# Optimization experiments

Measured on AMD Instinct MI355X. Metric: run time of the kernel, lower is better.

The kernel has to match this reference:

```python
import jax, jax.numpy as jnp
import numpy as np

N, E, B = 131072, 262144, 4096
NODE_DIM, EDGE_DIM, HIDDEN = 16, 4, 64
MLP_HID = 128


def setup_inputs() -> dict:
    key = jax.random.key(0)
    ks = jax.random.split(key, 16)
    def nrm(k, shape, s=0.05):
        return jax.random.normal(k, shape, jnp.float32) * s
    return {
        "x": jax.random.normal(ks[0], (N, NODE_DIM), jnp.float32),
        "edge_attr": jax.random.normal(ks[1], (E, EDGE_DIM), jnp.float32),
        "edge_index": jax.random.randint(ks[2], (2, E), 0, N),
        "batch": jnp.sort(jax.random.randint(ks[3], (N,), 0, B)),
        "w_e1": nrm(ks[4], (EDGE_DIM, MLP_HID)),
        "b_e1": jnp.zeros((MLP_HID,), jnp.float32),
        "w_e2": nrm(ks[5], (MLP_HID, NODE_DIM * HIDDEN)),
        "b_e2": jnp.zeros((NODE_DIM * HIDDEN,), jnp.float32),
        "root": nrm(ks[6], (NODE_DIM, HIDDEN)),
        "conv_bias": jnp.zeros((HIDDEN,), jnp.float32),
        "gru_wih": nrm(ks[7], (3 * HIDDEN, HIDDEN)),
        "gru_whh": nrm(ks[8], (3 * HIDDEN, HIDDEN)),
        "gru_bih": jnp.zeros((3 * HIDDEN,), jnp.float32),
        "gru_bhh": jnp.zeros((3 * HIDDEN,), jnp.float32),
        "lstm_wih": nrm(ks[9], (4 * HIDDEN, 2 * HIDDEN)),
        "lstm_whh": nrm(ks[10], (4 * HIDDEN, HIDDEN)),
        "lstm_bih": jnp.zeros((4 * HIDDEN,), jnp.float32),
        "lstm_bhh": jnp.zeros((4 * HIDDEN,), jnp.float32),
        "fc1_w": nrm(ks[11], (2 * HIDDEN, HIDDEN)),
        "fc1_b": jnp.zeros((HIDDEN,), jnp.float32),
        "fc2_w": nrm(ks[12], (HIDDEN, 1)),
        "fc2_b": jnp.zeros((1,), jnp.float32),
    }


def reference(x, edge_attr, edge_index, batch,
              w_e1, b_e1, w_e2, b_e2, root, conv_bias,
              gru_wih, gru_whh, gru_bih, gru_bhh,
              lstm_wih, lstm_whh, lstm_bih, lstm_bhh,
              fc1_w, fc1_b, fc2_w, fc2_b):
    src, dst = edge_index[0], edge_index[1]
    # NNConv: edge-MLP -> per-edge weight [E, node_dim, hidden]
    Wdyn = (jax.nn.relu(edge_attr @ w_e1 + b_e1) @ w_e2 + b_e2).reshape(E, NODE_DIM, HIDDEN)
    msg = jnp.einsum('ed,edh->eh', x[src], Wdyn)  # gather + per-edge matmul
    msum = jax.ops.segment_sum(msg, dst, num_segments=N)
    cnt = jax.ops.segment_sum(jnp.ones((E,), msg.dtype), dst, num_segments=N)
    agg = msum / jnp.maximum(cnt, 1.0)[:, None]  # scatter-mean
    out = jax.nn.relu(agg + x @ root + conv_bias)
    h = out
    for _ in range(3):
        gi = out @ gru_wih.T + gru_bih
        gh = h @ gru_whh.T + gru_bhh
        ir, iz, inn = jnp.split(gi, 3, axis=-1)
        hr, hz, hn = jnp.split(gh, 3, axis=-1)
        r = jax.nn.sigmoid(ir + hr)
        z = jax.nn.sigmoid(iz + hz)
        n = jnp.tanh(inn + r * hn)
        h = (1.0 - z) * n + z * h
        out = h
    # Set2Set, 3 processing steps
    hl = jnp.zeros((B, HIDDEN), out.dtype)
    cl = jnp.zeros((B, HIDDEN), out.dtype)
    q_star = jnp.zeros((B, 2 * HIDDEN), out.dtype)
    for _ in range(3):
        gates = q_star @ lstm_wih.T + lstm_bih + hl @ lstm_whh.T + lstm_bhh
        ig, fg, gg, og = jnp.split(gates, 4, axis=-1)
        ig = jax.nn.sigmoid(ig); fg = jax.nn.sigmoid(fg)
        gg = jnp.tanh(gg); og = jax.nn.sigmoid(og)
        cl = fg * cl + ig * gg
        hl = og * jnp.tanh(cl)
        q = hl  # [B, H]
        e = jnp.sum(out * q[batch], axis=-1)  # [N]
        m = jax.lax.stop_gradient(jax.ops.segment_max(e, batch, num_segments=B))
        ex = jnp.exp(e - m[batch])
        denom = jax.ops.segment_sum(ex, batch, num_segments=B)
        a = ex / denom[batch]  # segment softmax
        r_g = jax.ops.segment_sum(a[:, None] * out, batch, num_segments=B)
        q_star = jnp.concatenate([q, r_g], axis=-1)
    y = jax.nn.relu(q_star @ fc1_w + fc1_b)
    return (y @ fc2_w + fc2_b).squeeze(-1)
```

## Files before the change

### kernel.cpp

```cpp
#include <hip/hip_runtime.h>
#include <math.h>

#define N_NODES 131072
#define N_EDGES 262144
#define N_B     4096

typedef __attribute__((ext_vector_type(8))) short short8;
typedef __attribute__((ext_vector_type(8))) _Float16 half8;
typedef __attribute__((ext_vector_type(4))) float f32x4;
typedef __attribute__((ext_vector_type(16))) float f32x16;

__device__ __forceinline__ float fast_sig(float x) {
    return 1.0f / (1.0f + __expf(-x));
}
__device__ __forceinline__ float fast_tanh(float x) {
    float t = __expf(-2.0f * fabsf(x));
    float r = (1.0f - t) / (1.0f + t);
    return copysignf(r, x);
}

__device__ __forceinline__ void split_fp16(float v, _Float16& hi, _Float16& lo) {
    _Float16 h = (_Float16)v;
    hi = h;
    lo = (_Float16)(v - (float)h);
}

__global__ __launch_bounds__(256) void k_misc(
    const float* __restrict__ we2, unsigned short* __restrict__ wt,
    const float* __restrict__ gwih, const float* __restrict__ gwhh,
    const float* __restrict__ gbih, const float* __restrict__ gbhh,
    unsigned short* __restrict__ wtg, float* __restrict__ gbias,
    const float* __restrict__ lwih, const float* __restrict__ lwhh,
    float4* __restrict__ wA, float4* __restrict__ wB,
    const int* __restrict__ batch, int* __restrict__ starts,
    const int* __restrict__ eidx, int* __restrict__ deg)
{
    const int bid = blockIdx.x;
    const int tid = threadIdx.x;
    if (bid >= 105) {
        int p = (bid - 105) * 256 + tid;
        atomicAdd(&deg[eidx[N_EDGES + p]], 1);
        return;
    }
    if (bid < 64) {
        int p = bid * 256 + tid;
        int d = p >> 10;
        int u = (p >> 9) & 1;
        int s = (p >> 6) & 7;
        int l = p & 63;
        int k0 = s * 16 + ((l >> 5) << 3);
        int h = u * 32 + (l & 31);
        half8 hv;
        #pragma unroll
        for (int j = 0; j < 8; ++j) {
            float v = we2[(size_t)(k0 + j) * 1024 + d * 64 + h];
            hv[j] = (_Float16)v;
        }
        size_t base = (size_t)d * 8192 + (size_t)u * 4096 + s * 512 + l * 8;
        *(half8*)&wt[base] = hv;
    } else if (bid < 72) {
        int p = (bid - 64) * 256 + tid;
        if (p < 256) {
            int g = p >> 6, j = p & 63;
            float b;
            if (g == 0)      b = gbih[j] + gbhh[j];
            else if (g == 1) b = gbih[64 + j] + gbhh[64 + j];
            else if (g == 2) b = gbih[128 + j];
            else             b = gbhh[128 + j];
            gbias[p] = b;
        }
        int u = p >> 7, ks = (p >> 6) & 1, ln = p & 63;
        int n = u * 16 + (ln & 15);
        int g = n >> 6, jn = n & 63;
        int k0 = ks * 32 + (ln >> 4) * 8;
        half8 hv;
        #pragma unroll
        for (int jj = 0; jj < 8; ++jj) {
            int k = k0 + jj;
            float v;
            if (g == 0)      v = gwih[jn * 64 + k] + gwhh[jn * 64 + k];
            else if (g == 1) v = gwih[(64 + jn) * 64 + k] + gwhh[(64 + jn) * 64 + k];
            else if (g == 2) v = gwih[(128 + jn) * 64 + k];
            else             v = gwhh[(128 + jn) * 64 + k];
            hv[jj] = (_Float16)v;
        }
        size_t base = (size_t)(u * 2 + ks) * 512 + ln * 8;
        *(half8*)&wtg[base] = hv;
    } else if (bid < 88) {
        int p = (bid - 72) * 256 + tid;
        int k = p >> 6, ln = p & 63;
        float4 a, b;
        a.x = lwih[(0 * 64 + ln) * 128 + k] + lwhh[(0 * 64 + ln) * 64 + k];
        a.y = lwih[(1 * 64 + ln) * 128 + k] + lwhh[(1 * 64 + ln) * 64 + k];
        a.z = lwih[(2 * 64 + ln) * 128 + k] + lwhh[(2 * 64 + ln) * 64 + k];
        a.w = lwih[(3 * 64 + ln) * 128 + k] + lwhh[(3 * 64 + ln) * 64 + k];
        b.x = lwih[(0 * 64 + ln) * 128 + 64 + k];
        b.y = lwih[(1 * 64 + ln) * 128 + 64 + k];
        b.z = lwih[(2 * 64 + ln) * 128 + 64 + k];
        b.w = lwih[(3 * 64 + ln) * 128 + 64 + k];
        wA[p] = a; wB[p] = b;
    } else {
        int g = (bid - 88) * 256 + tid;
        if (g > N_B) return;
        if (g == N_B) { starts[N_B] = N_NODES; return; }
        int lo = 0, hi = N_NODES;
        while (lo < hi) {
            int mid = (lo + hi) >> 1;
            if (batch[mid] < g) lo = mid + 1; else hi = mid;
        }
        starts[g] = lo;
    }
}

__global__ __launch_bounds__(256) void k_scan1(
    const int* __restrict__ deg, int* __restrict__ psum)
{
    __shared__ int sm[256];
    const int t = threadIdx.x;
    sm[t] = deg[blockIdx.x * 256 + t];
    __syncthreads();
    #pragma unroll
    for (int off = 128; off; off >>= 1) {
        if (t < off) sm[t] += sm[t + off];
        __syncthreads();
    }
    if (t == 0) psum[blockIdx.x] = sm[0];
}

__global__ __launch_bounds__(512) void k_scan2(
    const int* __restrict__ psum, int* __restrict__ psumx)
{
    __shared__ int sm[512];
    const int t = threadIdx.x;
    sm[t] = psum[t];
    __syncthreads();
    #pragma unroll
    for (int off = 1; off < 512; off <<= 1) {
        int add = (t >= off) ? sm[t - off] : 0;
        __syncthreads();
        sm[t] += add;
        __syncthreads();
    }
    psumx[t] = (t > 0) ? sm[t - 1] : 0;
}

__global__ __launch_bounds__(256) void k_scan3(
    const int* __restrict__ deg, const int* __restrict__ psumx,
    int* __restrict__ row_ptr, int* __restrict__ cursor)
{
    __shared__ int sm[256];
    const int t = threadIdx.x;
    const int i = blockIdx.x * 256 + t;
    int d = deg[i];
    sm[t] = d;
    __syncthreads();
    #pragma unroll
    for (int off = 1; off < 256; off <<= 1) {
        int add = (t >= off) ? sm[t - off] : 0;
        __syncthreads();
        sm[t] += add;
        __syncthreads();
    }
    int excl = sm[t] - d + psumx[blockIdx.x];
    row_ptr[i] = excl;
    cursor[i] = excl;
    if (i == 0) row_ptr[N_NODES] = N_EDGES;
}

__global__ __launch_bounds__(256) void k_scat(
    const int* __restrict__ eidx, int* __restrict__ cursor,
    int* __restrict__ epos)
{
    int e = blockIdx.x * 256 + threadIdx.x;
    int dst = eidx[N_EDGES + e];
    epos[e] = atomicAdd(&cursor[dst], 1);
}

__global__ __launch_bounds__(512)
__attribute__((amdgpu_waves_per_eu(4, 8)))
void k_edge(
    const float* __restrict__ x,
    const float* __restrict__ ea,
    const int*   __restrict__ eidx,
    const int*   __restrict__ epos,
    const float* __restrict__ we1,
    const float* __restrict__ be1,
    const unsigned short* __restrict__ wt,
    const float* __restrict__ be2,
    float* __restrict__ emsg)
{
    __shared__ unsigned short sAh[16384];
    __shared__ float sxT[16 * 136];
    __shared__ float sbe2[1024];
    __shared__ int   spos[128];

    const int tid = threadIdx.x;
    const int w   = tid >> 6;
    const int ln  = tid & 63;
    const int u   = w >> 2;
    const int mt  = w & 3;
    const int eb  = blockIdx.x * 128;

    if (tid < 128) spos[tid] = epos[eb + tid];
    #pragma unroll
    for (int v = tid; v < 1024; v += 512) sbe2[v] = be2[v];

    {
        int e = tid >> 2, q = tid & 3;
        int src = eidx[eb + e];
        float4 t4 = ((const float4*)(x + (size_t)src * 16))[q];
        sxT[(q * 4 + 0) * 136 + e] = t4.x;
        sxT[(q * 4 + 1) * 136 + e] = t4.y;
        sxT[(q * 4 + 2) * 136 + e] = t4.z;
        sxT[(q * 4 + 3) * 136 + e] = t4.w;
    }

    #pragma unroll 1
    for (int i = 0; i < 4; ++i) {
        int cc = tid + i * 512;
        int mtc = cc >> 9;
        int s  = (cc >> 6) & 7;
        int l  = cc & 63;
        int e   = mtc * 32 + (l & 31);
        int kk0 = s * 16 + ((l >> 5) << 3);
        float4 eav = *(const float4*)(ea + (size_t)(eb + e) * 4);
        float4 b0 = *(const float4*)(be1 + kk0);
        float4 b1 = *(const float4*)(be1 + kk0 + 4);
        float acc[8] = {b0.x, b0.y, b0.z, b0.w, b1.x, b1.y, b1.z, b1.w};
        #pragma unroll
        for (int a = 0; a < 4; ++a) {
            float4 wa0 = *(const float4*)(we1 + a * 128 + kk0);
            float4 wa1 = *(const float4*)(we1 + a * 128 + kk0 + 4);
            float ev = (a == 0) ? eav.x : (a == 1) ? eav.y : (a == 2) ? eav.z : eav.w;
            acc[0] += ev * wa0.x; acc[1] += ev * wa0.y;
            acc[2] += ev * wa0.z; acc[3] += ev * wa0.w;
            acc[4] += ev * wa1.x; acc[5] += ev * wa1.y;
            acc[6] += ev * wa1.z; acc[7] += ev * wa1.w;
        }
        half8 hv;
        #pragma unroll
        for (int j = 0; j < 8; ++j) {
            hv[j] = (_Float16)fmaxf(acc[j], 0.0f);
        }
        *(half8*)&sAh[cc * 8] = hv;
    }
    __syncthreads();

    half8 ah[8];
    #pragma unroll
    for (int s = 0; s < 8; ++s) {
        ah[s] = *(half8*)&sAh[((mt * 8 + s) * 64 + ln) * 8];
    }
    #pragma unroll
    for (int s = 0; s < 8; ++s) {
        asm volatile("" : "+v"(ah[s]));
    }

    const unsigned short* wdu = wt + (size_t)u * 4096;
    const int d0 = blockIdx.x & 15;
    const int rbase = (ln >> 5) * 4;

    f32x16 msg;
    #pragma unroll
    for (int r = 0; r < 16; ++r) msg[r] = 0.0f;

    half8 bq[8];
    {
        const unsigned short* p0 = wdu + (size_t)d0 * 8192 + ln * 8;
        #pragma unroll
        for (int f = 0; f < 7; ++f) bq[f] = *(const half8*)(p0 + f * 512);
    }

    #pragma unroll 1
    for (int dd = 0; dd < 16; ++dd) {
        const int d = (d0 + dd) & 15;
        const unsigned short* wd  = wdu + (size_t)d * 8192;
        const unsigned short* wnx = wdu + (size_t)((d + 1) & 15) * 8192;

        float bv = sbe2[d * 64 + u * 32 + (ln & 31)];
        f32x16 c2;
        #pragma unroll
        for (int r = 0; r < 16; ++r) c2[r] = bv;

        #pragma unroll
        for (int s = 0; s < 8; ++s) {
            if (s == 0) {
                bq[7] = *(const half8*)(wd + 7 * 512 + ln * 8);
            } else if (dd < 15) {
                bq[s - 1] = *(const half8*)(wnx + (s - 1) * 512 + ln * 8);
            }
            c2 = __builtin_amdgcn_mfma_f32_32x32x16_f16(ah[s], bq[s], c2, 0, 0, 0);
        }
        #pragma unroll
        for (int q = 0; q < 4; ++q) {
            f32x4 xv = *(const f32x4*)&sxT[d * 136 + mt * 32 + rbase + 8 * q];
            #pragma unroll
            for (int j = 0; j < 4; ++j) {
                msg[q * 4 + j] = fmaf(xv[j], c2[q * 4 + j], msg[q * 4 + j]);
            }
        }
    }

    const int col = u * 32 + (ln & 31);
    #pragma unroll
    for (int r = 0; r < 16; ++r) {
        int row = (r & 3) + ((r >> 2) * 8) + rbase;
        int pos = spos[mt * 32 + row];
        emsg[(size_t)pos * 64 + col] = msg[r];
    }
}

__global__ __launch_bounds__(256, 2) void k_gru2(
    float* __restrict__ buf,
    const float* __restrict__ emsg,
    const int* __restrict__ rowp,
    const float* __restrict__ x,
    const float* __restrict__ root,
    const float* __restrict__ cb,
    const unsigned short* __restrict__ wtg,
    const float* __restrict__ gbias)
{
    __shared__ unsigned short sAh[16384];
    __shared__ unsigned short sAl[16384];
    __shared__ float sroot[1024];
    __shared__ float sbias[256];
    __shared__ float scb[64];
    const int tid = threadIdx.x;
    const int w = tid >> 6, ln = tid & 63, lq = ln >> 4, lm = ln & 15;
    const size_t nbase = (size_t)blockIdx.x * 256;

    #pragma unroll
    for (int v = tid; v < 1024; v += 256) sroot[v] = root[v];
    sbias[tid] = gbias[tid];
    if (tid < 64) scb[tid] = cb[tid];
    __syncthreads();

    #pragma unroll 2
    for (int i = 0; i < 8; ++i) {
        int cc = tid + i * 256;
        int mt = cc >> 7, ks = (cc >> 6) & 1, l = cc & 63;
        size_t gn = nbase + mt * 16 + (l & 15);
        int c0 = ks * 32 + (l >> 4) * 8;
        int rp0 = rowp[gn], rp1 = rowp[gn + 1];
        float ms[8] = {0.f, 0.f, 0.f, 0.f, 0.f, 0.f, 0.f, 0.f};
        for (int k = rp0; k < rp1; ++k) {
            float4 m0 = *(const float4*)(emsg + (size_t)k * 64 + c0);
            float4 m1 = *(const float4*)(emsg + (size_t)k * 64 + c0 + 4);
            ms[0] += m0.x; ms[1] += m0.y; ms[2] += m0.z; ms[3] += m0.w;
            ms[4] += m1.x; ms[5] += m1.y; ms[6] += m1.z; ms[7] += m1.w;
        }
        float cinv = 1.0f / fmaxf((float)(rp1 - rp0), 1.0f);
        float xv[16];
        *(float4*)&xv[0]  = *(const float4*)(x + gn * 16);
        *(float4*)&xv[4]  = *(const float4*)(x + gn * 16 + 4);
        *(float4*)&xv[8]  = *(const float4*)(x + gn * 16 + 8);
        *(float4*)&xv[12] = *(const float4*)(x + gn * 16 + 12);
        float acc[8];
        #pragma unroll
        for (int j = 0; j < 8; ++j) acc[j] = scb[c0 + j];
        #pragma unroll
        for (int d = 0; d < 16; ++d) {
            float xd = xv[d];
            #pragma unroll
            for (int j = 0; j < 8; ++j) acc[j] += xd * sroot[d * 64 + c0 + j];
        }
        half8 hv, lv;
        #pragma unroll
        for (int j = 0; j < 8; ++j) {
            float hval = fmaxf(ms[j] * cinv + acc[j], 0.0f);
            _Float16 hi, lo; split_fp16(hval, hi, lo);
            hv[j] = hi; lv[j] = lo;
        }
        *(half8*)&sAh[cc * 8] = hv;
        *(half8*)&sAl[cc * 8] = lv;
    }
    __syncthreads();

    #pragma unroll 1
    for (int step = 0; step < 3; ++step) {
        half8 ah[4][2], al[4][2];
        #pragma unroll
        for (int i = 0; i < 4; ++i)
            #pragma unroll
            for (int ks = 0; ks < 2; ++ks) {
                int mt = w * 4 + i;
                ah[i][ks] = *(half8*)&sAh[((mt * 2 + ks) * 64 + ln) * 8];
                al[i][ks] = *(half8*)&sAl[((mt * 2 + ks) * 64 + ln) * 8];
            }
        __syncthreads();

        #pragma unroll 1
        for (int v = 0; v < 4; ++v) {
            f32x4 C[4][4];
            #pragma unroll
            for (int g = 0; g < 4; ++g) {
                float bv = sbias[g * 64 + v * 16 + lm];
                #pragma unroll
                for (int i = 0; i < 4; ++i) C[g][i] = (f32x4){bv, bv, bv, bv};
            }
            #pragma unroll
            for (int g = 0; g < 4; ++g) {
                int u = g * 4 + v;
                #pragma unroll
                for (int ks = 0; ks < 2; ++ks) {
                    size_t wb = (size_t)(u * 2 + ks) * 512 + ln * 8;
                    half8 bb = *(const half8*)&wtg[wb];
                    #pragma unroll
                    for (int i = 0; i < 4; ++i) {
                        C[g][i] = __builtin_amdgcn_mfma_f32_16x16x32_f16(ah[i][ks], bb, C[g][i], 0, 0, 0);
                        C[g][i] = __builtin_amdgcn_mfma_f32_16x16x32_f16(al[i][ks], bb, C[g][i], 0, 0, 0);
                    }
                }
            }
            int ksp = v >> 1;
            int lq2 = (v & 1) * 2 + (lm >> 3);
            int jp = lm & 7;
            #pragma unroll
            for (int i = 0; i < 4; ++i) {
                int mt = w * 4 + i;
                #pragma unroll
                for (int r = 0; r < 4; ++r) {
                    int idx = ((mt * 2 + ksp) * 64 + lq2 * 16 + lq * 4 + r) * 8 + jp;
                    float hold = (float)*(const _Float16*)&sAh[idx]
                               + (float)*(const _Float16*)&sAl[idx];
                    float rr = fast_sig(C[0][i][r]);
                    float zz = fast_sig(C[1][i][r]);
                    float nn = fast_tanh(C[2][i][r] + rr * C[3][i][r]);
                    float hnew = (1.0f - zz) * nn + zz * hold;
                    if (step < 2) {
                        _Float16 hi, lo; split_fp16(hnew, hi, lo);
                        sAh[idx] = *(unsigned short*)&hi;
                        sAl[idx] = *(unsigned short*)&lo;
                    } else {
                        buf[(nbase + mt * 16 + lq * 4 + r) * 64 + v * 16 + lm] = hnew;
                    }
                }
            }
        }
        if (step < 2) __syncthreads();
    }
}

__global__ __launch_bounds__(256) void k_s2s(
    const float* __restrict__ out,
    const int*   __restrict__ starts,
    const float4* __restrict__ wA,
    const float4* __restrict__ wB,
    const float* __restrict__ bih,
    const float* __restrict__ bhh,
    const float* __restrict__ fc1w,
    const float* __restrict__ fc1b,
    const float* __restrict__ fc2w,
    const float* __restrict__ fc2b,
    float* __restrict__ y)
{
    __shared__ float osh[4][32][66];
    __shared__ float qsL[4][128];
    __shared__ float ebuf[4][256];
    const int tid = threadIdx.x;
    const int wv = tid >> 6, ln = tid & 63;
    const int gid = blockIdx.x * 4 + wv;

    const int s0 = starts[gid];
    int L = starts[gid + 1] - s0; if (L > 256) L = 256;
    const int SL = (L < 32) ? L : 32;

    #pragma unroll
    for (int base = 0; base < 32; base += 4) {
        int row = base + (ln >> 4);
        int c4 = (ln & 15) * 4;
        if (row < SL)
            *(float4*)&osh[wv][row][c4] =
                *(const float4*)(out + (size_t)(s0 + row) * 64 + c4);
    }

    qsL[wv][ln] = 0.0f; qsL[wv][64 + ln] = 0.0f;
    __builtin_amdgcn_wave_barrier();

    const float b0 = bih[ln] + bhh[ln];
    const float b1 = bih[64 + ln] + bhh[64 + ln];
    const float b2 = bih[128 + ln] + bhh[128 + ln];
    const float b3 = bih[192 + ln] + bhh[192 + ln];

    float c = 0.0f;

    #pragma unroll 1
    for (int step = 0; step < 3; ++step) {
        float a0 = b0, a1 = b1, a2 = b2, a3 = b3;
        #pragma unroll 4
        for (int k = 0; k < 64; ++k) {
            float qk = qsL[wv][k];
            float rk = qsL[wv][64 + k];
            float4 wa = wA[k * 64 + ln];
            float4 wb = wB[k * 64 + ln];
            a0 += wa.x * qk + wb.x * rk;
            a1 += wa.y * qk + wb.y * rk;
            a2 += wa.z * qk + wb.z * rk;
            a3 += wa.w * qk + wb.w * rk;
        }
        float ig = fast_sig(a0), fg = fast_sig(a1);
        float gg = fast_tanh(a2), og = fast_sig(a3);
        c = fg * c + ig * gg;
        float h = og * fast_tanh(c);
        __builtin_amdgcn_wave_barrier();
        qsL[wv][ln] = h;
        __builtin_amdgcn_wave_barrier();

        float m = -1e30f;
        for (int c0 = 0; c0 * 64 < L; ++c0) {
            int j = c0 * 64 + ln;
            if (j < L) {
                float a = 0.0f;
                if (j < SL) {
                    #pragma unroll
                    for (int l4 = 0; l4 < 16; ++l4) {
                        float4 ov = *(const float4*)&osh[wv][j][l4 * 4];
                        float4 hv = *(const float4*)&qsL[wv][l4 * 4];
                        a += ov.x * hv.x + ov.y * hv.y + ov.z * hv.z + ov.w * hv.w;
                    }
                } else {
                    const float4* orow = (const float4*)(out + (size_t)(s0 + j) * 64);
                    #pragma unroll
                    for (int l4 = 0; l4 < 16; ++l4) {
                        float4 ov = orow[l4];
                        float4 hv = *(const float4*)&qsL[wv][l4 * 4];
                        a += ov.x * hv.x + ov.y * hv.y + ov.z * hv.z + ov.w * hv.w;
                    }
                }
                ebuf[wv][j] = a;
                m = fmaxf(m, a);
            }
        }
        #pragma unroll
        for (int off = 32; off; off >>= 1) m = fmaxf(m, __shfl_xor(m, off));
        float ds = 0.0f;
        for (int c0 = 0; c0 * 64 < L; ++c0) {
            int j = c0 * 64 + ln;
            if (j < L) {
                float ex = __expf(ebuf[wv][j] - m);
                ebuf[wv][j] = ex;
                ds += ex;
            }
        }
        #pragma unroll
        for (int off = 32; off; off >>= 1) ds += __shfl_xor(ds, off);
        __builtin_amdgcn_wave_barrier();
        float rg = 0.0f;
        for (int j = 0; j < SL; ++j)
            rg = fmaf(ebuf[wv][j], osh[wv][j][ln], rg);
        for (int j = SL; j < L; ++j)
            rg = fmaf(ebuf[wv][j], out[(size_t)(s0 + j) * 64 + ln], rg);
        rg = (L > 0) ? (rg / ds) : 0.0f;
        qsL[wv][64 + ln] = rg;
        __builtin_amdgcn_wave_barrier();
    }

    float a = fc1b[ln];
    #pragma unroll 4
    for (int k = 0; k < 128; ++k)
        a = fmaf(qsL[wv][k], fc1w[k * 64 + ln], a);
    float uu = fmaxf(a, 0.0f) * fc2w[ln];
    #pragma unroll
    for (int off = 32; off; off >>= 1) uu += __shfl_xor(uu, off);
    if (ln == 0) y[gid] = uu + fc2b[0];
}

extern "C" void kernel_launch(void* const* d_in, const int* in_sizes, int n_in,
                              void* d_out, int out_size, void* d_ws, size_t ws_size,
                              hipStream_t stream) {
    const float* x     = (const float*)d_in[0];
    const float* ea    = (const float*)d_in[1];
    const int*   eidx  = (const int*)d_in[2];
    const int*   batch = (const int*)d_in[3];
    const float* we1   = (const float*)d_in[4];
    const float* be1   = (const float*)d_in[5];
    const float* we2   = (const float*)d_in[6];
    const float* be2   = (const float*)d_in[7];
    const float* root  = (const float*)d_in[8];
    const float* cb    = (const float*)d_in[9];
    const float* gwih  = (const float*)d_in[10];
    const float* gwhh  = (const float*)d_in[11];
    const float* gbih  = (const float*)d_in[12];
    const float* gbhh  = (const float*)d_in[13];
    const float* lwih  = (const float*)d_in[14];
    const float* lwhh  = (const float*)d_in[15];
    const float* lbih  = (const float*)d_in[16];
    const float* lbhh  = (const float*)d_in[17];
    const float* fc1w  = (const float*)d_in[18];
    const float* fc1b  = (const float*)d_in[19];
    const float* fc2w  = (const float*)d_in[20];
    const float* fc2b  = (const float*)d_in[21];

    float* emsg = (float*)d_ws;
    float* buf  = emsg + (size_t)N_EDGES * 64;
    int* deg    = (int*)(buf + (size_t)N_NODES * 64);
    int* cursor = deg + N_NODES;
    int* rowp   = cursor + N_NODES;
    int* epos   = rowp + N_NODES + 1;
    int* psum   = epos + N_EDGES;
    int* psumx  = psum + 512;
    int* starts = psumx + 512;
    size_t off = (size_t)((char*)(starts + N_B + 1) - (char*)d_ws);
    off = (off + 15) & ~(size_t)15;
    unsigned short* wt  = (unsigned short*)((char*)d_ws + off);
    unsigned short* wtg = wt + 262144;
    float* gbias = (float*)(wtg + 32768);
    float4* wA = (float4*)(gbias + 256);
    float4* wB = wA + 4096;
    float* y = (float*)d_out;

    hipMemsetAsync(deg, 0, (size_t)N_NODES * sizeof(int), stream);
    k_misc<<<1129, 256, 0, stream>>>(we2, wt, gwih, gwhh, gbih, gbhh, wtg, gbias,
                                     lwih, lwhh, wA, wB, batch, starts, eidx, deg);
    k_scan1<<<512, 256, 0, stream>>>(deg, psum);
    k_scan2<<<1, 512, 0, stream>>>(psum, psumx);
    k_scan3<<<512, 256, 0, stream>>>(deg, psumx, rowp, cursor);
    k_scat<<<1024, 256, 0, stream>>>(eidx, cursor, epos);
    k_edge<<<N_EDGES / 128, 512, 0, stream>>>(x, ea, eidx, epos, we1, be1, wt, be2, emsg);
    k_gru2<<<N_NODES / 256, 256, 0, stream>>>(buf, emsg, rowp, x, root, cb,
                                              wtg, gbias);
    k_s2s<<<N_B / 4, 256, 0, stream>>>(buf, starts, wA, wB, lbih, lbhh,
                                       fc1w, fc1b, fc2w, fc2b, y);
}
```

Measured before the change: 369.1 us.

## Stage edge-MLP weight slices in LDS with double-buffered async global loads

```diff
diff --git a/kernel.cpp b/kernel.cpp
--- a/kernel.cpp
+++ b/kernel.cpp
@@ -23,6 +23,12 @@
     _Float16 h = (_Float16)v;
     hi = h;
     lo = (_Float16)(v - (float)h);
+}
+
+__device__ __forceinline__ void load_lds16(const void* g, void* l) {
+    __builtin_amdgcn_global_load_lds(
+        (const __attribute__((address_space(1))) unsigned int*)g,
+        (__attribute__((address_space(3))) unsigned int*)l, 16, 0, 0);
 }
 
 __global__ __launch_bounds__(256) void k_misc(
@@ -190,6 +196,7 @@
     float* __restrict__ emsg)
 {
     __shared__ unsigned short sAh[16384];
+    __shared__ unsigned short sB[2][8192];
     __shared__ float sxT[16 * 136];
     __shared__ float sbe2[1024];
     __shared__ int   spos[128];
@@ -200,6 +207,14 @@
     const int u   = w >> 2;
     const int mt  = w & 3;
     const int eb  = blockIdx.x * 128;
+    const int d0  = blockIdx.x & 15;
+
+    #pragma unroll
+    for (int r = 0; r < 2; ++r) {
+        int seg = r * 8 + w;
+        load_lds16(wt + (size_t)d0 * 8192 + seg * 512 + ln * 8,
+                   &sB[0][seg * 512]);
+    }
 
     if (tid < 128) spos[tid] = epos[eb + tid];
     #pragma unroll
@@ -256,26 +271,26 @@
         asm volatile("" : "+v"(ah[s]));
     }
 
-    const unsigned short* wdu = wt + (size_t)u * 4096;
-    const int d0 = blockIdx.x & 15;
     const int rbase = (ln >> 5) * 4;
 
     f32x16 msg;
     #pragma unroll
     for (int r = 0; r < 16; ++r) msg[r] = 0.0f;
-
-    half8 bq[8];
-    {
-        const unsigned short* p0 = wdu + (size_t)d0 * 8192 + ln * 8;
-        #pragma unroll
-        for (int f = 0; f < 7; ++f) bq[f] = *(const half8*)(p0 + f * 512);
-    }
 
     #pragma unroll 1
     for (int dd = 0; dd < 16; ++dd) {
         const int d = (d0 + dd) & 15;
-        const unsigned short* wd  = wdu + (size_t)d * 8192;
-        const unsigned short* wnx = wdu + (size_t)((d + 1) & 15) * 8192;
+        const int cur = dd & 1;
+
+        if (dd < 15) {
+            int dn = (d + 1) & 15;
+            #pragma unroll
+            for (int r = 0; r < 2; ++r) {
+                int seg = r * 8 + w;
+                load_lds16(wt + (size_t)dn * 8192 + seg * 512 + ln * 8,
+                           &sB[cur ^ 1][seg * 512]);
+            }
+        }
 
         float bv = sbe2[d * 64 + u * 32 + (ln & 31)];
         f32x16 c2;
@@ -284,12 +299,8 @@
 
         #pragma unroll
         for (int s = 0; s < 8; ++s) {
-            if (s == 0) {
-                bq[7] = *(const half8*)(wd + 7 * 512 + ln * 8);
-            } else if (dd < 15) {
-                bq[s - 1] = *(const half8*)(wnx + (s - 1) * 512 + ln * 8);
-            }
-            c2 = __builtin_amdgcn_mfma_f32_32x32x16_f16(ah[s], bq[s], c2, 0, 0, 0);
+            half8 bb = *(half8*)&sB[cur][u * 4096 + s * 512 + ln * 8];
+            c2 = __builtin_amdgcn_mfma_f32_32x32x16_f16(ah[s], bb, c2, 0, 0, 0);
         }
         #pragma unroll
         for (int q = 0; q < 4; ++q) {
@@ -299,6 +310,7 @@
                 msg[q * 4 + j] = fmaf(xv[j], c2[q * 4 + j], msg[q * 4 + j]);
             }
         }
+        __syncthreads();
     }
 
     const int col = u * 32 + (ln & 31);
```

New measurement: 367.0 us. Within noise of the previous version (-0.6%).
